# Kernel tuning notes

Hardware: AMD Instinct MI355X
Metric: run time of the kernel (lower is better)

Reference implementation:

```python
import jax, jax.numpy as jnp
import numpy as np

B, EMB, HID, OUT = 4096, 128, 512, 64
N_SUBPOLICIES = 5
STEPS = N_SUBPOLICIES * 4


def setup_inputs() -> dict:
    key = jax.random.key(0)
    ks = jax.random.split(key, 8)
    s = lambda k, shape: (jax.random.normal(k, shape, jnp.float32) * 0.05)
    return {
        "x": jax.random.randint(ks[0], (B,), 0, OUT),          # initial tokens
        "embedding": s(ks[1], (OUT, EMB)),                      # nn.Embedding weight
        "W_ih": s(ks[2], (4 * HID, EMB)),                       # LSTM input weights (i,f,g,o)
        "W_hh": s(ks[3], (4 * HID, HID)),                       # LSTM recurrent weights
        "b_ih": s(ks[4], (4 * HID,)),
        "b_hh": s(ks[5], (4 * HID,)),
        "W_lin": s(ks[6], (OUT, HID)),                          # nn.Linear weight
        "b_lin": s(ks[7], (OUT,)),
    }


def reference(x, embedding, W_ih, W_hh, b_ih, b_hh, W_lin, b_lin):
    keys = jax.random.split(jax.random.key(42), STEPS)
    h0 = jnp.zeros((x.shape[0], HID), jnp.float32)
    c0 = jnp.zeros_like(h0)
    b = b_ih + b_hh  # fold both LSTM biases once

    def step(carry, k):
        tok, h, c = carry
        e = embedding[tok]                               # [B, EMB]
        gates = e @ W_ih.T + h @ W_hh.T + b              # [B, 4H], torch gate order i,f,g,o
        i, f, g, o = jnp.split(gates, 4, axis=-1)
        c = jax.nn.sigmoid(f) * c + jax.nn.sigmoid(i) * jnp.tanh(g)
        h = jax.nn.sigmoid(o) * jnp.tanh(c)
        logits = h @ W_lin.T + b_lin                     # [B, OUT]
        probs = jax.nn.softmax(logits, axis=-1)
        # torch.multinomial(probs, 1) == categorical sample from logits
        new_tok = jax.random.categorical(k, logits, axis=-1)
        return (new_tok, h, c), probs

    _, probs = jax.lax.scan(step, (x, h0, c0), keys)     # [STEPS, B, OUT]
    return jnp.transpose(probs, (1, 0, 2))               # [B, STEPS, OUT]
```

## Files before the change

kernel.cpp:

```cpp
#include <hip/hip_runtime.h>
#include <stdint.h>
#include <math.h>


#define B_SZ  4096
#define EMB   128
#define HID   512
#define NOUT  64
#define STEPS 20
#define G4    2048
#define HF    ((size_t)B_SZ * HID)

typedef __attribute__((ext_vector_type(8)))  short bf16x8;
typedef __attribute__((ext_vector_type(16))) float f32x16;

__device__ __forceinline__ void tf2x32(uint32_t k0, uint32_t k1,
                                       uint32_t x0, uint32_t x1,
                                       uint32_t& o0, uint32_t& o1) {
  const uint32_t ks2 = k0 ^ k1 ^ 0x1BD11BDAu;
#define TFR(r) { x0 += x1; x1 = (x1 << (r)) | (x1 >> (32 - (r))); x1 ^= x0; }
  x0 += k0; x1 += k1;
  TFR(13) TFR(15) TFR(26) TFR(6)
  x0 += k1;  x1 += ks2 + 1u;
  TFR(17) TFR(29) TFR(16) TFR(24)
  x0 += ks2; x1 += k0 + 2u;
  TFR(13) TFR(15) TFR(26) TFR(6)
  x0 += k0;  x1 += k1 + 3u;
  TFR(17) TFR(29) TFR(16) TFR(24)
  x0 += k1;  x1 += ks2 + 4u;
  TFR(13) TFR(15) TFR(26) TFR(6)
  x0 += ks2; x1 += k0 + 5u;
#undef TFR
  o0 = x0; o1 = x1;
}

__device__ __forceinline__ void bf16split(float f, ushort& hi, ushort& lo) {
  uint32_t u = __float_as_uint(f);
  uint32_t r = u + 0x7fffu + ((u >> 16) & 1u);
  hi = (ushort)(r >> 16);
  float fh = __uint_as_float((r >> 16) << 16);
  float fl = f - fh;
  uint32_t v = __float_as_uint(fl);
  uint32_t r2 = v + 0x7fffu + ((v >> 16) & 1u);
  lo = (ushort)(r2 >> 16);
}

__device__ __forceinline__ void gload_lds16(const ushort* g, ushort* d) {
  __builtin_amdgcn_global_load_lds(
      (const __attribute__((address_space(1))) void*)g,
      (__attribute__((address_space(3))) void*)d, 16, 0, 0);
}

__global__ __launch_bounds__(256) void eproj_kernel(
    const float* __restrict__ emb, const float* __restrict__ W_ih,
    const float* __restrict__ b_ih, const float* __restrict__ b_hh,
    float* __restrict__ E) {
  const int t = blockIdx.x;
  __shared__ float es[EMB];
  for (int k = threadIdx.x; k < EMB; k += blockDim.x) es[k] = emb[t * EMB + k];
  __syncthreads();
  for (int j = threadIdx.x; j < G4; j += blockDim.x) {
    const float* w = W_ih + (size_t)j * EMB;
    float acc = 0.f;
#pragma unroll 8
    for (int k = 0; k < EMB; k += 4) {
      float4 wv = *(const float4*)(w + k);
      acc += wv.x * es[k] + wv.y * es[k + 1] + wv.z * es[k + 2] + wv.w * es[k + 3];
    }
    E[(size_t)t * G4 + j] = acc + b_ih[j] + b_hh[j];
  }
}

__global__ __launch_bounds__(256) void wprep_whh(
    const float* __restrict__ W_hh, ushort* __restrict__ wswz) {
  const int id = blockIdx.x * 256 + threadIdx.x;
  const int ub    = id >> 14;
  const int w14   = id & 16383;
  const int kt    = w14 >> 11;
  const int plane = (w14 >> 10) & 1;
  const int row   = (w14 >> 3) & 127;
  const int ec    = w14 & 7;
  const int grow = (row >> 5) * HID + ub * 32 + (row & 31);
  const int swz = (row & 7) << 3;
  ushort vals[8];
#pragma unroll
  for (int j = 0; j < 8; ++j) {
    const int e = ec * 8 + j;
    const int k = kt * 64 + (e ^ swz);
    ushort hi, lo;
    bf16split(W_hh[(size_t)grow * HID + k], hi, lo);
    vals[j] = plane ? lo : hi;
  }
  *(uint4*)(wswz + (size_t)id * 8) = *(const uint4*)vals;
}

__global__ __launch_bounds__(256) void wprep_lin(
    const float* __restrict__ W_lin, float* __restrict__ wlt) {
  const int id = blockIdx.x * 256 + threadIdx.x;
  const int j = id & 3, o = (id >> 2) & 63, k4 = id >> 8;
  wlt[id] = W_lin[(size_t)o * HID + k4 * 4 + j];
}

__global__ __launch_bounds__(256, 2) void lstm_step_mfma(
    const ushort* __restrict__ hf,
    float*        __restrict__ c,
    float*        __restrict__ h_out,
    ushort*       __restrict__ hf_out,
    const ushort* __restrict__ wswz,
    const float*  __restrict__ E,
    const int*    __restrict__ tok)
{
  __shared__ ushort Bt[2][16384];
  const int tid = threadIdx.x;
  const int w = tid >> 6, l = tid & 63;
  const int l31 = l & 31, lh = l >> 5;

  const int raw = blockIdx.x;
  const int x = raw & 7, j = raw >> 3;
  const int ub  = (x & 1) * 8 + (j & 7);
  const int mbi = (x >> 1) * 8 + (j >> 3);
  const int m0 = mbi * 128 + w * 32;
  const int u0 = ub * 32;

  f32x16 acc[4] = {};

  const size_t abase = ((size_t)(m0 >> 5) * 64 + lh) * 256 + (size_t)l31 * 8;
  const ushort* a0 = hf + abase;
  const ushort* a1 = hf + HF + abase;

  const ushort* wbase = wswz + (size_t)ub * 131072;

  {
    const ushort* src = wbase + (size_t)(w * 64 + l) * 8;
    ushort* dst = &Bt[0][w * 512];
#pragma unroll
    for (int r = 0; r < 8; ++r)
      gload_lds16(src + r * 2048, dst + r * 2048);
  }
  asm volatile("s_waitcnt vmcnt(0)" ::: "memory");
  __syncthreads();

  int buf = 0;
  for (int kt = 0; kt < 8; ++kt) {
    if (kt < 7) {
      const ushort* src = wbase + (size_t)(kt + 1) * 16384 + (size_t)(w * 64 + l) * 8;
      ushort* dst = &Bt[buf ^ 1][w * 512];
#pragma unroll
      for (int r = 0; r < 8; ++r)
        gload_lds16(src + r * 2048, dst + r * 2048);
    }
    bf16x8 A0[4], A1[4];
#pragma unroll
    for (int kc = 0; kc < 4; ++kc) {
      const size_t koff = (size_t)(kt * 8 + kc * 2) * 256;
      A0[kc] = *(const bf16x8*)(a0 + koff);
      A1[kc] = *(const bf16x8*)(a1 + koff);
    }
#pragma unroll
    for (int kc = 0; kc < 4; ++kc) {
#pragma unroll
      for (int s = 0; s < 4; ++s) {
        const int row = s * 32 + l31;
        const int phys = (((kc * 2 + lh) ^ (row & 7)) << 3);
        const ushort* rb = &Bt[buf][row * 64 + phys];
        const bf16x8 Bh = *(const bf16x8*)rb;
        const bf16x8 Bl = *(const bf16x8*)(rb + 8192);
        acc[s] = __builtin_amdgcn_mfma_f32_32x32x16_bf16(A0[kc], Bh, acc[s], 0, 0, 0);
        acc[s] = __builtin_amdgcn_mfma_f32_32x32x16_bf16(A1[kc], Bh, acc[s], 0, 0, 0);
        acc[s] = __builtin_amdgcn_mfma_f32_32x32x16_bf16(A0[kc], Bl, acc[s], 0, 0, 0);
      }
    }
    asm volatile("s_waitcnt vmcnt(0)" ::: "memory");
    __syncthreads();
    buf ^= 1;
  }

  const int u = u0 + l31;
#pragma unroll
  for (int r = 0; r < 16; ++r) {
    const int m = m0 + (r & 3) + 8 * (r >> 2) + 4 * lh;
    const int tk = tok[m];
    const float* Erow = E + (size_t)tk * G4;
    const float gi = acc[0][r] + Erow[u];
    const float gf = acc[1][r] + Erow[HID + u];
    const float gg = acc[2][r] + Erow[2 * HID + u];
    const float go = acc[3][r] + Erow[3 * HID + u];
    const float si = 1.f / (1.f + expf(-gi));
    const float sf = 1.f / (1.f + expf(-gf));
    const float so = 1.f / (1.f + expf(-go));
    const size_t ci = (size_t)m * HID + u;
    const float nc = sf * c[ci] + si * tanhf(gg);
    const float hv = so * tanhf(nc);
    c[ci] = nc;
    h_out[ci] = hv;
    ushort hi, lo;
    bf16split(hv, hi, lo);
    const size_t fo = ((size_t)(m >> 5) * 64 + (u >> 3)) * 256 + (size_t)(m & 31) * 8 + (u & 7);
    hf_out[fo] = hi;
    hf_out[HF + fo] = lo;
  }
}

__global__ __launch_bounds__(256) void logits2(
    const float* __restrict__ h, const float* __restrict__ wlt,
    const float* __restrict__ b_lin, float* __restrict__ out,
    int* __restrict__ tok, int step)
{
  const int tid = threadIdx.x;
  const int o = tid & 63;
  const int rg = tid >> 6;
  const int b0 = blockIdx.x * 8 + rg * 2;
  float acc0 = 0.f, acc1 = 0.f;
  const float* h0 = h + (size_t)b0 * HID;
  const float* h1 = h0 + HID;
#pragma unroll 4
  for (int k4 = 0; k4 < 128; ++k4) {
    const float4 wv = *(const float4*)(wlt + (size_t)(k4 * 64 + o) * 4);
    const float4 x0 = *(const float4*)(h0 + k4 * 4);
    const float4 x1 = *(const float4*)(h1 + k4 * 4);
    acc0 += wv.x * x0.x + wv.y * x0.y + wv.z * x0.z + wv.w * x0.w;
    acc1 += wv.x * x1.x + wv.y * x1.y + wv.z * x1.z + wv.w * x1.w;
  }
  const float bl = b_lin[o];
  uint32_t s0, s1;
  tf2x32(0u, 42u, 0u, (uint32_t)step, s0, s1);
  float lg[2] = {acc0 + bl, acc1 + bl};
#pragma unroll
  for (int r = 0; r < 2; ++r) {
    const int b = b0 + r;
    const float logit = lg[r];
    float mx = logit;
#pragma unroll
    for (int d = 32; d; d >>= 1) mx = fmaxf(mx, __shfl_xor(mx, d));
    float e = expf(logit - mx);
    float ssum = e;
#pragma unroll
    for (int d = 32; d; d >>= 1) ssum += __shfl_xor(ssum, d);
    out[((size_t)b * STEPS + step) * NOUT + o] = e / ssum;

    uint32_t r0, r1;
    tf2x32(s0, s1, 0u, (uint32_t)(b * NOUT + o), r0, r1);
    const uint32_t bits = r0 ^ r1;
    float uu = __uint_as_float((bits >> 9) | 0x3f800000u) - 1.0f;
    uu = fmaxf(uu, 1.17549435e-38f);
    const float gmb = -logf(-logf(uu));
    float v = logit + gmb;
    int bi = o;
#pragma unroll
    for (int d = 32; d; d >>= 1) {
      float ov = __shfl_xor(v, d);
      int oi = __shfl_xor(bi, d);
      if (ov > v || (ov == v && oi < bi)) { v = ov; bi = oi; }
    }
    if (o == 0) tok[b] = bi;
  }
}

extern "C" void kernel_launch(void* const* d_in, const int* in_sizes, int n_in,
                              void* d_out, int out_size, void* d_ws, size_t ws_size,
                              hipStream_t stream) {
  const int*   x     = (const int*)d_in[0];
  const float* emb   = (const float*)d_in[1];
  const float* W_ih  = (const float*)d_in[2];
  const float* W_hh  = (const float*)d_in[3];
  const float* b_ih  = (const float*)d_in[4];
  const float* b_hh  = (const float*)d_in[5];
  const float* W_lin = (const float*)d_in[6];
  const float* b_lin = (const float*)d_in[7];
  float* out = (float*)d_out;

  float*  E    = (float*)d_ws;
  float*  c    = E + 131072;
  float*  h    = c + HF;
  float*  wlt  = h + HF;
  ushort* hf0  = (ushort*)(wlt + 32768);
  ushort* hf1  = hf0 + 2 * HF;
  ushort* wswz = hf1 + 2 * HF;
  int*    tok  = (int*)(wswz + 2097152);

  hipMemsetAsync(hf0, 0, 2 * HF * sizeof(ushort), stream);
  hipMemsetAsync(c, 0, HF * sizeof(float), stream);

  eproj_kernel<<<64, 256, 0, stream>>>(emb, W_ih, b_ih, b_hh, E);
  wprep_whh<<<1024, 256, 0, stream>>>(W_hh, wswz);
  wprep_lin<<<128, 256, 0, stream>>>(W_lin, wlt);

  const int* cur_tok = x;
  ushort* hfin = hf0;
  ushort* hfout = hf1;
  for (int t = 0; t < STEPS; ++t) {
    lstm_step_mfma<<<512, 256, 0, stream>>>(hfin, c, h, hfout, wswz, E, cur_tok);
    logits2<<<512, 256, 0, stream>>>(h, wlt, b_lin, out, tok, t);
    cur_tok = tok;
    ushort* tmp = hfin; hfin = hfout; hfout = tmp;
  }
}
```

Before: 1.318 ms.

## Enlarge LSTM step tiles to 512 threads with pipelined staging and skip zero-state step

The LSTM step kernel now runs 256 blocks of 512 threads, each covering 256 batch rows, so every W_hh tile staged into LDS is reused across twice as many rows. The K loop is fully unrolled into a software pipeline that prefetches the next weight stage and A fragments while computing the current one, using partial vmcnt waits, sched barriers and raised wave priority during MFMA. The LDS swizzle changes to a 4-element granularity read as two 8-byte halves to alter bank conflict behaviour. The first step skips the GEMM and the c load because h and c are zero, which removes the two memsets. In exchange the kernel needs more registers per thread for the double A buffers, and each wave carries more in-flight loads.

```diff
diff --git a/kernel.cpp b/kernel.cpp
--- a/kernel.cpp
+++ b/kernel.cpp
@@ -13,6 +13,8 @@
 
 typedef __attribute__((ext_vector_type(8)))  short bf16x8;
 typedef __attribute__((ext_vector_type(16))) float f32x16;
+
+union B8 { uint2 q[2]; bf16x8 v; };
 
 __device__ __forceinline__ void tf2x32(uint32_t k0, uint32_t k1,
                                        uint32_t x0, uint32_t x1,
@@ -81,7 +83,7 @@
   const int row   = (w14 >> 3) & 127;
   const int ec    = w14 & 7;
   const int grow = (row >> 5) * HID + ub * 32 + (row & 31);
-  const int swz = (row & 7) << 3;
+  const int swz = (row & 15) << 2;
   ushort vals[8];
 #pragma unroll
   for (int j = 0; j < 8; ++j) {
@@ -101,14 +103,15 @@
   wlt[id] = W_lin[(size_t)o * HID + k4 * 4 + j];
 }
 
-__global__ __launch_bounds__(256, 2) void lstm_step_mfma(
+__global__ __launch_bounds__(512, 2) void lstm_step_mfma(
     const ushort* __restrict__ hf,
     float*        __restrict__ c,
     float*        __restrict__ h_out,
     ushort*       __restrict__ hf_out,
     const ushort* __restrict__ wswz,
     const float*  __restrict__ E,
-    const int*    __restrict__ tok)
+    const int*    __restrict__ tok,
+    int zh)
 {
   __shared__ ushort Bt[2][16384];
   const int tid = threadIdx.x;
@@ -117,9 +120,9 @@
 
   const int raw = blockIdx.x;
   const int x = raw & 7, j = raw >> 3;
-  const int ub  = (x & 1) * 8 + (j & 7);
-  const int mbi = (x >> 1) * 8 + (j >> 3);
-  const int m0 = mbi * 128 + w * 32;
+  const int ub  = (x & 3) * 4 + (j & 3);
+  const int mbi = (x >> 2) * 8 + (j >> 2);
+  const int m0 = mbi * 256 + w * 32;
   const int u0 = ub * 32;
 
   f32x16 acc[4] = {};
@@ -127,52 +130,66 @@
   const size_t abase = ((size_t)(m0 >> 5) * 64 + lh) * 256 + (size_t)l31 * 8;
   const ushort* a0 = hf + abase;
   const ushort* a1 = hf + HF + abase;
-
-  const ushort* wbase = wswz + (size_t)ub * 131072;
-
-  {
-    const ushort* src = wbase + (size_t)(w * 64 + l) * 8;
-    ushort* dst = &Bt[0][w * 512];
-#pragma unroll
-    for (int r = 0; r < 8; ++r)
-      gload_lds16(src + r * 2048, dst + r * 2048);
-  }
-  asm volatile("s_waitcnt vmcnt(0)" ::: "memory");
-  __syncthreads();
-
-  int buf = 0;
-  for (int kt = 0; kt < 8; ++kt) {
-    if (kt < 7) {
-      const ushort* src = wbase + (size_t)(kt + 1) * 16384 + (size_t)(w * 64 + l) * 8;
-      ushort* dst = &Bt[buf ^ 1][w * 512];
-#pragma unroll
-      for (int r = 0; r < 8; ++r)
-        gload_lds16(src + r * 2048, dst + r * 2048);
-    }
-    bf16x8 A0[4], A1[4];
-#pragma unroll
-    for (int kc = 0; kc < 4; ++kc) {
-      const size_t koff = (size_t)(kt * 8 + kc * 2) * 256;
-      A0[kc] = *(const bf16x8*)(a0 + koff);
-      A1[kc] = *(const bf16x8*)(a1 + koff);
-    }
-#pragma unroll
-    for (int kc = 0; kc < 4; ++kc) {
-#pragma unroll
-      for (int s = 0; s < 4; ++s) {
-        const int row = s * 32 + l31;
-        const int phys = (((kc * 2 + lh) ^ (row & 7)) << 3);
-        const ushort* rb = &Bt[buf][row * 64 + phys];
-        const bf16x8 Bh = *(const bf16x8*)rb;
-        const bf16x8 Bl = *(const bf16x8*)(rb + 8192);
-        acc[s] = __builtin_amdgcn_mfma_f32_32x32x16_bf16(A0[kc], Bh, acc[s], 0, 0, 0);
-        acc[s] = __builtin_amdgcn_mfma_f32_32x32x16_bf16(A1[kc], Bh, acc[s], 0, 0, 0);
-        acc[s] = __builtin_amdgcn_mfma_f32_32x32x16_bf16(A0[kc], Bl, acc[s], 0, 0, 0);
-      }
-    }
-    asm volatile("s_waitcnt vmcnt(0)" ::: "memory");
-    __syncthreads();
-    buf ^= 1;
+  const ushort* wsrc = wswz + (size_t)ub * 131072 + (size_t)(w * 512 + l * 8);
+
+  if (!zh) {
+    bf16x8 Aa0[4], Aa1[4], Ab0[4], Ab1[4];
+
+#define SB0 __builtin_amdgcn_sched_barrier(0)
+#define STAGE(KT, BUF) { \
+  _Pragma("unroll") \
+  for (int r = 0; r < 4; ++r) \
+    gload_lds16(wsrc + (size_t)(KT) * 16384 + r * 4096, &Bt[BUF][w * 512 + r * 4096]); }
+#define LOADA(KT, A0v, A1v) { \
+  _Pragma("unroll") \
+  for (int kc = 0; kc < 4; ++kc) { \
+    const size_t ko = (size_t)((KT) * 8 + kc * 2) * 256; \
+    A0v[kc] = *(const bf16x8*)(a0 + ko); \
+    A1v[kc] = *(const bf16x8*)(a1 + ko); } }
+#define COMPUTE(BUF, A0v, A1v) { \
+  __builtin_amdgcn_s_setprio(1); \
+  _Pragma("unroll") \
+  for (int kc = 0; kc < 4; ++kc) { \
+    _Pragma("unroll") \
+    for (int s = 0; s < 4; ++s) { \
+      const int row = s * 32 + l31; \
+      const int swz = (row & 15) << 2; \
+      const int eb = kc * 16 + lh * 8; \
+      const ushort* rb = &Bt[BUF][row * 64]; \
+      B8 uh, ul; \
+      uh.q[0] = *(const uint2*)(rb + ((eb)     ^ swz)); \
+      uh.q[1] = *(const uint2*)(rb + ((eb + 4) ^ swz)); \
+      ul.q[0] = *(const uint2*)(rb + 8192 + ((eb)     ^ swz)); \
+      ul.q[1] = *(const uint2*)(rb + 8192 + ((eb + 4) ^ swz)); \
+      acc[s] = __builtin_amdgcn_mfma_f32_32x32x16_bf16(A0v[kc], uh.v, acc[s], 0, 0, 0); \
+      acc[s] = __builtin_amdgcn_mfma_f32_32x32x16_bf16(A1v[kc], uh.v, acc[s], 0, 0, 0); \
+      acc[s] = __builtin_amdgcn_mfma_f32_32x32x16_bf16(A0v[kc], ul.v, acc[s], 0, 0, 0); } } \
+  __builtin_amdgcn_s_setprio(0); }
+#define FENCE8 { asm volatile("s_waitcnt vmcnt(8)" ::: "memory"); SB0; \
+                 __builtin_amdgcn_s_barrier(); }
+
+    STAGE(0, 0); SB0; LOADA(0, Aa0, Aa1); SB0;
+    FENCE8;
+    STAGE(1, 1); SB0; LOADA(1, Ab0, Ab1); SB0;
+    COMPUTE(0, Aa0, Aa1); FENCE8;
+    STAGE(2, 0); SB0; LOADA(2, Aa0, Aa1); SB0;
+    COMPUTE(1, Ab0, Ab1); FENCE8;
+    STAGE(3, 1); SB0; LOADA(3, Ab0, Ab1); SB0;
+    COMPUTE(0, Aa0, Aa1); FENCE8;
+    STAGE(4, 0); SB0; LOADA(4, Aa0, Aa1); SB0;
+    COMPUTE(1, Ab0, Ab1); FENCE8;
+    STAGE(5, 1); SB0; LOADA(5, Ab0, Ab1); SB0;
+    COMPUTE(0, Aa0, Aa1); FENCE8;
+    STAGE(6, 0); SB0; LOADA(6, Aa0, Aa1); SB0;
+    COMPUTE(1, Ab0, Ab1); FENCE8;
+    STAGE(7, 1); SB0; LOADA(7, Ab0, Ab1); SB0;
+    COMPUTE(0, Aa0, Aa1); FENCE8;
+    COMPUTE(1, Ab0, Ab1);
+#undef FENCE8
+#undef COMPUTE
+#undef LOADA
+#undef STAGE
+#undef SB0
   }
 
   const int u = u0 + l31;
@@ -189,7 +206,8 @@
     const float sf = 1.f / (1.f + expf(-gf));
     const float so = 1.f / (1.f + expf(-go));
     const size_t ci = (size_t)m * HID + u;
-    const float nc = sf * c[ci] + si * tanhf(gg);
+    const float cv = zh ? 0.f : c[ci];
+    const float nc = sf * cv + si * tanhf(gg);
     const float hv = so * tanhf(nc);
     c[ci] = nc;
     h_out[ci] = hv;
@@ -278,9 +296,6 @@
   ushort* wswz = hf1 + 2 * HF;
   int*    tok  = (int*)(wswz + 2097152);
 
-  hipMemsetAsync(hf0, 0, 2 * HF * sizeof(ushort), stream);
-  hipMemsetAsync(c, 0, HF * sizeof(float), stream);
-
   eproj_kernel<<<64, 256, 0, stream>>>(emb, W_ih, b_ih, b_hh, E);
   wprep_whh<<<1024, 256, 0, stream>>>(W_hh, wswz);
   wprep_lin<<<128, 256, 0, stream>>>(W_lin, wlt);
@@ -289,7 +304,7 @@
   ushort* hfin = hf0;
   ushort* hfout = hf1;
   for (int t = 0; t < STEPS; ++t) {
-    lstm_step_mfma<<<512, 256, 0, stream>>>(hfin, c, h, hfout, wswz, E, cur_tok);
+    lstm_step_mfma<<<256, 512, 0, stream>>>(hfin, c, h, hfout, wswz, E, cur_tok, t == 0);
     logits2<<<512, 256, 0, stream>>>(h, wlt, b_lin, out, tok, t);
     cur_tok = tok;
     ushort* tmp = hfin; hfin = hfout; hfout = tmp;
```

Result: no change. 1.326 ms (+0.6%).
